# Optimization experiments

Hardware: AMD Instinct MI355X
Metric: run time of the kernel (lower is better)

Reference implementation:

```python
import jax, jax.numpy as jnp
import numpy as np
from jax import lax

A_NUM = 3
STRIDES = (4, 8, 16, 32, 64)
LEVEL_HW = ((128, 208), (64, 104), (32, 52), (16, 26), (8, 13))
IMG_H, IMG_W = 512.0, 832.0
PRE_NMS, POST_NMS, NMS_TH = 6000, 1000, 0.7


def _base_anchors(base_size, ratios=(0.5, 1.0, 2.0), scales=(8.0,)):
    ratios = np.asarray(ratios, np.float64)
    scales = np.asarray(scales, np.float64)
    cx = cy = (base_size - 1) / 2.0
    size = float(base_size) * float(base_size)
    ws = np.round(np.sqrt(size / ratios))
    hs = np.round(ws * ratios)
    ws = (ws[:, None] * scales[None, :]).reshape(-1)
    hs = (hs[:, None] * scales[None, :]).reshape(-1)
    return np.stack([cx - 0.5 * (ws - 1), cy - 0.5 * (hs - 1),
                     cx + 0.5 * (ws - 1), cy + 0.5 * (hs - 1)], axis=1)


def _all_anchors():
    # generate_anchors_global: per-level shifted grids, concatenated, order (h, w, a)
    out = []
    for stride, (h, w) in zip(STRIDES, LEVEL_HW):
        base = _base_anchors(stride)  # [A,4]
        sx = np.arange(w) * stride
        sy = np.arange(h) * stride
        sx, sy = np.meshgrid(sx, sy)
        shifts = np.stack([sx.ravel(), sy.ravel(), sx.ravel(), sy.ravel()], axis=1)
        anc = (shifts[:, None, :] + base[None, :, :]).reshape(-1, 4)  # [H*W*A,4]
        out.append(anc)
    return np.concatenate(out, axis=0).astype(np.float32)

_ANCHORS = _all_anchors()


def _conv(x, w, b, pad):
    y = lax.conv_general_dilated(x, w, (1, 1), [(pad, pad), (pad, pad)],
                                 dimension_numbers=('NCHW', 'OIHW', 'NCHW'))
    return y + b[None, :, None, None]


def _bbox_transform_inv(anchors, deltas):
    w = anchors[:, 2] - anchors[:, 0] + 1.0
    h = anchors[:, 3] - anchors[:, 1] + 1.0
    cx = anchors[:, 0] + 0.5 * w
    cy = anchors[:, 1] + 0.5 * h
    dx, dy, dw, dh = deltas[:, 0], deltas[:, 1], deltas[:, 2], deltas[:, 3]
    pcx = dx * w + cx
    pcy = dy * h + cy
    pw = jnp.exp(dw) * w
    ph = jnp.exp(dh) * h
    return jnp.stack([pcx - 0.5 * pw, pcy - 0.5 * ph,
                      pcx + 0.5 * pw, pcy + 0.5 * ph], axis=1)


def _iou_one_to_many(box, boxes):
    area = (boxes[:, 2] - boxes[:, 0] + 1.0) * (boxes[:, 3] - boxes[:, 1] + 1.0)
    area_b = (box[2] - box[0] + 1.0) * (box[3] - box[1] + 1.0)
    xx1 = jnp.maximum(box[0], boxes[:, 0])
    yy1 = jnp.maximum(box[1], boxes[:, 1])
    xx2 = jnp.minimum(box[2], boxes[:, 2])
    yy2 = jnp.minimum(box[3], boxes[:, 3])
    iw = jnp.maximum(0.0, xx2 - xx1 + 1.0)
    ih = jnp.maximum(0.0, yy2 - yy1 + 1.0)
    inter = iw * ih
    return inter / (area + area_b - inter)


def _nms_fixed(boxes, scores, thresh, max_out):
    # greedy NMS with a fixed number of iterations (jit-friendly)
    def body(s, _):
        i = jnp.argmax(s)
        valid = s[i] > -jnp.inf
        ious = _iou_one_to_many(boxes[i], boxes)
        s2 = jnp.where(ious > thresh, -jnp.inf, s)
        s2 = s2.at[i].set(-jnp.inf)
        return s2, (i, valid)
    _, (idx, valid) = lax.scan(body, scores, None, length=max_out)
    return idx, valid


def _rpn_forward(feats, im_info, rpn_conv_w, rpn_conv_b, rpn_score_w,
                 rpn_score_b, rpn_bbox_w, rpn_bbox_b):
    fg_scores, bbox_deltas = [], []
    for p in feats:
        H, W = p.shape[-2], p.shape[-1]
        f = _conv(p, rpn_conv_w, rpn_conv_b, 1)              # [1,512,H,W]
        cls = _conv(f, rpn_score_w, rpn_score_b, 0)          # [1,2A,H,W]
        # _reshape_layer(.,2) + softmax(dim=1) + _reshape_layer back + permute
        prob = jax.nn.softmax(cls.reshape(1, 2, A_NUM, H, W), axis=1)
        prob = prob.reshape(1, 2 * A_NUM, H, W).transpose(0, 2, 3, 1)  # [1,H,W,2A]
        fg = prob[..., A_NUM:].reshape(-1)                    # fg prob, order (h,w,a)
        bb = _conv(f, rpn_bbox_w, rpn_bbox_b, 0).transpose(0, 2, 3, 1).reshape(-1, 4)
        fg_scores.append(fg)
        bbox_deltas.append(bb)
    scores = jnp.concatenate(fg_scores, axis=0)              # [Ntot]
    deltas = jnp.concatenate(bbox_deltas, axis=0)            # [Ntot,4]
    anchors = jnp.asarray(_ANCHORS)

    proposals = _bbox_transform_inv(anchors, deltas)
    # clip to image
    proposals = jnp.stack([
        jnp.clip(proposals[:, 0], 0.0, im_info[1] - 1.0),
        jnp.clip(proposals[:, 1], 0.0, im_info[0] - 1.0),
        jnp.clip(proposals[:, 2], 0.0, im_info[1] - 1.0),
        jnp.clip(proposals[:, 3], 0.0, im_info[0] - 1.0)], axis=1)

    # pre-NMS top-k by score
    top_scores, order = lax.top_k(scores, PRE_NMS)
    top_boxes = proposals[order]
    keep, valid = _nms_fixed(top_boxes, top_scores, NMS_TH, POST_NMS)
    vmask = valid.astype(top_boxes.dtype)[:, None]
    sel_boxes = top_boxes[keep] * vmask
    sel_scores = top_scores[keep][:, None] * vmask
    rois = jnp.concatenate([jnp.zeros((POST_NMS, 1), sel_boxes.dtype), sel_boxes], axis=1)
    return jnp.concatenate([rois, sel_scores], axis=1)        # [POST_NMS, 6]


def setup_inputs() -> dict:
    key = jax.random.key(0)
    ks = jax.random.split(key, 12)
    chans = 256
    feats = {}
    for i, (name, (h, w)) in enumerate(zip(['p2', 'p3', 'p4', 'p5', 'p6'], LEVEL_HW)):
        feats[name] = jax.random.normal(ks[i], (1, chans, h, w), jnp.float32)
    inp = dict(feats)
    inp['im_info'] = jnp.array([IMG_H, IMG_W, 1.0], jnp.float32)
    inp['rpn_conv_w'] = jax.random.normal(ks[5], (512, chans, 3, 3), jnp.float32) * 0.03
    inp['rpn_conv_b'] = jnp.zeros((512,), jnp.float32)
    inp['rpn_score_w'] = jax.random.normal(ks[6], (2 * A_NUM, 512, 1, 1), jnp.float32) * 0.03
    inp['rpn_score_b'] = jnp.zeros((2 * A_NUM,), jnp.float32)
    inp['rpn_bbox_w'] = jax.random.normal(ks[7], (4 * A_NUM, 512, 1, 1), jnp.float32) * 0.01
    inp['rpn_bbox_b'] = jnp.zeros((4 * A_NUM,), jnp.float32)
    return inp


def reference(p2, p3, p4, p5, p6, im_info, rpn_conv_w, rpn_conv_b,
              rpn_score_w, rpn_score_b, rpn_bbox_w, rpn_bbox_b):
    return _rpn_forward([p2, p3, p4, p5, p6], im_info, rpn_conv_w, rpn_conv_b,
                        rpn_score_w, rpn_score_b, rpn_bbox_w, rpn_bbox_b)
```

## Files before the change

kernel.cpp:

```cpp
#include <hip/hip_runtime.h>
#include <stdint.h>

#define N_ANCH   106392
#define PRE_NMS  6000
#define POST_NMS 1000
#define POOL_CAP 8192
#define NMS_BLKS 94
#define SUP_W    96

static __device__ const int    LV_H[5]      = {128, 64, 32, 16, 8};
static __device__ const int    LV_W[5]      = {208, 104, 52, 26, 13};
static __device__ const int    LV_STRIDE[5] = {4, 8, 16, 32, 64};
static __device__ const int    LV_PIX[5]    = {26624, 6656, 1664, 416, 104};
static __device__ const int    LV_TILE0[6]  = {0, 416, 520, 546, 553, 555};
static __device__ const int    LV_AOFF[6]   = {0, 79872, 99840, 104832, 106080, 106392};
static __device__ const int    GPOFF[6]     = {0, 26624, 33280, 34944, 35360, 35464};
static __device__ const double BASE_ANCH[5][3][4] = {
  {{-22.,-10.,25.,13.},   {-14.,-14.,17.,17.},    {-10.,-22.,13.,25.}},
  {{-40.,-20.,47.,27.},   {-28.,-28.,35.,35.},    {-20.,-44.,27.,51.}},
  {{-84.,-40.,99.,55.},   {-56.,-56.,71.,71.},    {-36.,-80.,51.,95.}},
  {{-164.,-72.,195.,103.},{-112.,-112.,143.,143.},{-76.,-168.,107.,199.}},
  {{-332.,-152.,395.,215.},{-224.,-224.,287.,287.},{-148.,-328.,211.,391.}}
};

__device__ __forceinline__ uint32_t sort32f(float f) {
  uint32_t u = __float_as_uint(f);
  return ((int)u < 0) ? ~u : (u | 0x80000000u);
}
__device__ __forceinline__ uint64_t sort64(double d) {
  uint64_t u = (uint64_t)__double_as_longlong(d);
  return ((long long)u < 0) ? ~u : (u | 0x8000000000000000ull);
}

__device__ __forceinline__ double combf(const float* sw, const float* bw, int c, int j) {
  if (j < 3) return (double)sw[(3 + j) * 512 + c] - (double)sw[j * 512 + c];
  return (double)bw[(j - 3) * 512 + c];
}

__global__ __launch_bounds__(256) void k_weff_part(const float* __restrict__ cw,
                                                   const float* __restrict__ sw,
                                                   const float* __restrict__ bw,
                                                   double* __restrict__ Wpart) {
  int chunk = blockIdx.x / 9;
  int tb = blockIdx.x % 9;
  int t = tb * 256 + threadIdx.x;
  int c0 = chunk * 32;
  double acc[15];
#pragma unroll
  for (int j = 0; j < 15; ++j) acc[j] = 0.0;
#pragma unroll 1
  for (int c = c0; c < c0 + 32; ++c) {
    double v = (double)cw[c * 2304 + t];
#pragma unroll
    for (int j = 0; j < 15; ++j) acc[j] += v * combf(sw, bw, c, j);
  }
  double* o = Wpart + (((size_t)chunk * 2304 + t) << 4);
#pragma unroll
  for (int j = 0; j < 15; ++j) o[j] = acc[j];
  o[15] = 0.0;
}

__global__ __launch_bounds__(256) void k_weff_fin(const double* __restrict__ Wpart,
                                                  const float* __restrict__ cb,
                                                  const float* __restrict__ sb,
                                                  const float* __restrict__ bb,
                                                  const float* __restrict__ sw,
                                                  const float* __restrict__ bw,
                                                  double* __restrict__ Weff,
                                                  double* __restrict__ fb,
                                                  float4* __restrict__ w3,
                                                  float* __restrict__ fb32) {
  if (blockIdx.x == 9) {
    __shared__ double ps[15][16];
    int tid = threadIdx.x;
    if (tid < 240) {
      int j = tid >> 4, part = tid & 15;
      double s = 0.0;
      for (int c = part * 32; c < part * 32 + 32; ++c)
        s += (double)cb[c] * combf(sw, bw, c, j);
      ps[j][part] = s;
    }
    __syncthreads();
    if (tid < 15) {
      double s = 0.0;
#pragma unroll
      for (int part = 0; part < 16; ++part) s += ps[tid][part];
      s += (tid < 3) ? ((double)sb[3 + tid] - (double)sb[tid]) : (double)bb[tid - 3];
      fb[tid] = s;
      if (tid < 3) fb32[tid] = (float)s;
    }
    if (tid == 15) fb32[3] = 0.f;
    return;
  }
  int t = blockIdx.x * 256 + threadIdx.x;
  double acc[15];
#pragma unroll
  for (int j = 0; j < 15; ++j) acc[j] = 0.0;
#pragma unroll 1
  for (int chunk = 0; chunk < 16; ++chunk) {
    const double* p = Wpart + (((size_t)chunk * 2304 + t) << 4);
#pragma unroll
    for (int j = 0; j < 15; ++j) acc[j] += p[j];
  }
  double* o = Weff + ((size_t)t << 4);
#pragma unroll
  for (int j = 0; j < 15; ++j) o[j] = acc[j];
  o[15] = 0.0;
  float4 wf;
  wf.x = (float)acc[0]; wf.y = (float)acc[1]; wf.z = (float)acc[2]; wf.w = 0.f;
  w3[t] = wf;
}

__device__ __forceinline__ void load9(float v[9], const float* __restrict__ ib,
                                      const bool rok[3], const bool cok[3],
                                      const int roff[3]) {
#pragma unroll
  for (int ky = 0; ky < 3; ++ky)
#pragma unroll
    for (int kx = 0; kx < 3; ++kx)
      v[ky * 3 + kx] = (rok[ky] && cok[kx]) ? ib[roff[ky] + kx] : 0.0f;
}

__global__ __launch_bounds__(256) void k_fast(
    const float* __restrict__ p0, const float* __restrict__ p1,
    const float* __restrict__ p2, const float* __restrict__ p3,
    const float* __restrict__ p4,
    const float4* __restrict__ w3, const float* __restrict__ fb32,
    float* __restrict__ logits32, uint32_t* __restrict__ hist) {
  __shared__ float4 w3s[2304];
  __shared__ float red[4][64][3];
  int tid = threadIdx.x, wv = tid >> 6, ln = tid & 63;
  for (int i = tid; i < 2304; i += 256) w3s[i] = w3[i];
  int t = blockIdx.x;
  int L = 0;
  while (L < 4 && t >= LV_TILE0[L + 1]) ++L;
  const float* inL = (L == 0) ? p0 : (L == 1) ? p1 : (L == 2) ? p2 : (L == 3) ? p3 : p4;
  int H = LV_H[L], W = LV_W[L], HW = H * W, PIX = LV_PIX[L];
  int pix = (t - LV_TILE0[L]) * 64 + ln;
  bool valid = pix < PIX;
  if (!valid) pix = PIX - 1;
  int h = pix / W, w = pix % W;
  bool rok[3], cok[3];
  int roff[3];
#pragma unroll
  for (int ky = 0; ky < 3; ++ky) {
    int iy = h + ky - 1;
    rok[ky] = (iy >= 0 && iy < H);
    roff[ky] = iy * W + w - 1;
  }
#pragma unroll
  for (int kx = 0; kx < 3; ++kx) {
    int ix = w + kx - 1;
    cok[kx] = (ix >= 0 && ix < W);
  }
  __syncthreads();
  float a0 = 0.f, a1 = 0.f, a2 = 0.f;
  int ci0 = wv * 64;
  const float* ib = inL + ci0 * HW;
#pragma unroll 1
  for (int ci = ci0; ci < ci0 + 64; ++ci, ib += HW) {
    float v[9];
    load9(v, ib, rok, cok, roff);
    const float4* wr = w3s + ci * 9;
#pragma unroll
    for (int t9 = 0; t9 < 9; ++t9) {
      float4 wt = wr[t9];
      float vv = v[t9];
      a0 += vv * wt.x; a1 += vv * wt.y; a2 += vv * wt.z;
    }
  }
  red[wv][ln][0] = a0; red[wv][ln][1] = a1; red[wv][ln][2] = a2;
  __syncthreads();
  if (wv == 0 && valid) {
    int gbase = LV_AOFF[L] + pix * 3;
#pragma unroll
    for (int a = 0; a < 3; ++a) {
      float f = (red[0][ln][a] + red[1][ln][a]) + (red[2][ln][a] + red[3][ln][a]);
      f += fb32[a];
      logits32[gbase + a] = f;
      atomicAdd(&hist[sort32f(f) >> 16], 1u);
    }
  }
}

__global__ __launch_bounds__(1024) void k_edge(const uint32_t* __restrict__ hist,
                                               uint32_t* __restrict__ cnts) {
  __shared__ uint32_t cs[1024];
  __shared__ uint32_t g_grp, g_suf;
  int t = threadIdx.x, wv = t >> 6, ln = t & 63;
#pragma unroll 4
  for (int r = 0; r < 64; ++r) {
    int g = r * 16 + wv;
    uint32_t x = hist[g * 64 + ln];
#pragma unroll
    for (int off = 32; off > 0; off >>= 1) x += __shfl_down(x, off);
    if (ln == 0) cs[g] = x;
  }
  __syncthreads();
  for (int off = 1; off < 1024; off <<= 1) {
    uint32_t v = cs[t] + ((t + off < 1024) ? cs[t + off] : 0u);
    __syncthreads();
    cs[t] = v;
    __syncthreads();
  }
  uint32_t sufnext = (t < 1023) ? cs[t + 1] : 0u;
  if (cs[t] >= PRE_NMS && sufnext < PRE_NMS) {
    g_grp = (uint32_t)t;
    g_suf = sufnext;
  }
  __syncthreads();
  if (t < 64) {
    uint32_t grp = g_grp, suf = g_suf;
    uint32_t x = hist[grp * 64 + t];
    uint32_t S = x;
#pragma unroll
    for (int off = 1; off < 64; off <<= 1) {
      uint32_t y = __shfl_down(S, off);
      if (t + off < 64) S += y;
    }
    unsigned long long mask = __ballot(suf + S >= PRE_NMS);
    int hi = 63 - (int)__clzll(mask);
    if (t == hi) {
      uint32_t e = grp * 64 + (uint32_t)hi;
      cnts[1] = (e > 2) ? e - 2 : 0;
    }
  }
}

__global__ __launch_bounds__(256) void k_compact(const float* __restrict__ logits32,
                                                 uint32_t* __restrict__ cnts,
                                                 uint32_t* __restrict__ alist) {
  int i = blockIdx.x * 256 + threadIdx.x;
  if (i >= N_ANCH) return;
  if ((sort32f(logits32[i]) >> 16) >= cnts[1]) {
    uint32_t pos = atomicAdd(&cnts[0], 1u);
    if (pos < POOL_CAP) alist[pos] = (uint32_t)i;
  }
}

__global__ __launch_bounds__(256) void k_refine(
    const float* __restrict__ p0, const float* __restrict__ p1,
    const float* __restrict__ p2, const float* __restrict__ p3,
    const float* __restrict__ p4,
    const double* __restrict__ Weff, const double* __restrict__ fb,
    const uint32_t* __restrict__ alist, const uint32_t* __restrict__ cnts,
    double* __restrict__ logits, double* __restrict__ deltas,
    uint64_t* __restrict__ pkey) {
  __shared__ double red[4][64][5];
  int tid = threadIdx.x, wv = tid >> 6, ln = tid & 63;
  int cnt = (int)cnts[0];
  if (cnt > POOL_CAP) cnt = POOL_CAP;
  int base = blockIdx.x * 64;
  if (base >= cnt) return;
  int slot = base + ln;
  if (slot >= cnt) slot = cnt - 1;
  int gi = (int)alist[slot];
  int gpix = gi / 3, a = gi - gpix * 3;
  int L = 0;
  while (L < 4 && gpix >= GPOFF[L + 1]) ++L;
  int pix = gpix - GPOFF[L];
  const float* inL = (L == 0) ? p0 : (L == 1) ? p1 : (L == 2) ? p2 : (L == 3) ? p3 : p4;
  int H = LV_H[L], W = LV_W[L], HW = H * W;
  int h = pix / W, w = pix % W;
  bool rok[3], cok[3];
  int roff[3];
#pragma unroll
  for (int ky = 0; ky < 3; ++ky) {
    int iy = h + ky - 1;
    rok[ky] = (iy >= 0 && iy < H);
    roff[ky] = iy * W + w - 1;
  }
#pragma unroll
  for (int kx = 0; kx < 3; ++kx) {
    int ix = w + kx - 1;
    cok[kx] = (ix >= 0 && ix < W);
  }
  double sc = 0.0, d0 = 0.0, d1 = 0.0, d2 = 0.0, d3 = 0.0;
  int js = a, jd = 3 + 4 * a;
  int ci0 = wv * 64;
  const float* ib = inL + ci0 * HW;
#pragma unroll 1
  for (int ci = ci0; ci < ci0 + 64; ++ci, ib += HW) {
    float v[9];
    load9(v, ib, rok, cok, roff);
    const double* wr = Weff + ((size_t)ci * 144);
#pragma unroll
    for (int t9 = 0; t9 < 9; ++t9) {
      double vd = (double)v[t9];
      const double* wt = wr + t9 * 16;
      sc += vd * wt[js];
      d0 += vd * wt[jd + 0];
      d1 += vd * wt[jd + 1];
      d2 += vd * wt[jd + 2];
      d3 += vd * wt[jd + 3];
    }
  }
  red[wv][ln][0] = sc;
  red[wv][ln][1] = d0; red[wv][ln][2] = d1;
  red[wv][ln][3] = d2; red[wv][ln][4] = d3;
  __syncthreads();
  if (wv == 0) {
    double f[5];
#pragma unroll
    for (int j = 0; j < 5; ++j)
      f[j] = red[0][ln][j] + red[1][ln][j] + red[2][ln][j] + red[3][ln][j];
    double lg = f[0] + fb[js];
    logits[gi] = lg;
    deltas[gi * 4 + 0] = f[1] + fb[jd + 0];
    deltas[gi * 4 + 1] = f[2] + fb[jd + 1];
    deltas[gi * 4 + 2] = f[3] + fb[jd + 2];
    deltas[gi * 4 + 3] = f[4] + fb[jd + 3];
    pkey[slot] = (sort64(lg) & ~0x1FFFFull) | (uint64_t)(0x1FFFFu - (uint32_t)gi);
  }
}

__global__ __launch_bounds__(256) void k_rank_cnt(const uint32_t* __restrict__ cnts,
                                                  const uint64_t* __restrict__ pkey,
                                                  uint32_t* __restrict__ rank32) {
  __shared__ uint64_t lk[512];
  int t = threadIdx.x;
  int cnt = (int)cnts[0];
  if (cnt > POOL_CAP) cnt = POOL_CAP;
  int it = blockIdx.x >> 4, jc = blockIdx.x & 15;
  int e = it * 256 + t;
  int c0 = jc * 512;
  if (it * 256 >= cnt || c0 >= cnt) return;
  int lim = cnt - c0; if (lim > 512) lim = 512;
  for (int i = t; i < 512; i += 256) lk[i] = (i < lim) ? pkey[c0 + i] : 0ull;
  __syncthreads();
  bool active = e < cnt;
  uint64_t mykey = active ? pkey[e] : ~0ull;
  int r = 0;
#pragma unroll 8
  for (int j = 0; j < 512; ++j) r += (lk[j] > mykey) ? 1 : 0;
  if (active && r) atomicAdd(&rank32[e], (uint32_t)r);
}

__global__ __launch_bounds__(256) void k_scatter(const uint32_t* __restrict__ cnts,
                                                 const uint64_t* __restrict__ pkey,
                                                 const uint32_t* __restrict__ rank32,
                                                 const double* __restrict__ logits,
                                                 const double* __restrict__ deltas,
                                                 const float* __restrict__ im_info,
                                                 double* __restrict__ ss,
                                                 double* __restrict__ sbx,
                                                 float4* __restrict__ bxf,
                                                 float* __restrict__ areaf) {
  int t = threadIdx.x;
  int cnt = (int)cnts[0];
  if (cnt > POOL_CAP) cnt = POOL_CAP;
  int e = blockIdx.x * 256 + t;
  if (blockIdx.x * 256 >= cnt) return;
  if (e >= cnt) return;
  int rank = (int)rank32[e];
  if (rank >= PRE_NMS) return;
  uint64_t mykey = pkey[e];
  int gi = 0x1FFFF - (int)(mykey & 0x1FFFFull);
  int L = 0;
  while (L < 4 && gi >= LV_AOFF[L + 1]) ++L;
  int rel = gi - LV_AOFF[L];
  int pix = rel / 3, a = rel % 3;
  int W = LV_W[L];
  int h = pix / W, w = pix % W;
  double imW1 = (double)im_info[1] - 1.0;
  double imH1 = (double)im_info[0] - 1.0;
  double shx = (double)(w * LV_STRIDE[L]), shy = (double)(h * LV_STRIDE[L]);
  double ax1 = BASE_ANCH[L][a][0] + shx, ay1 = BASE_ANCH[L][a][1] + shy;
  double ax2 = BASE_ANCH[L][a][2] + shx, ay2 = BASE_ANCH[L][a][3] + shy;
  double dx = deltas[gi * 4 + 0], dy = deltas[gi * 4 + 1];
  double dw = deltas[gi * 4 + 2], dh = deltas[gi * 4 + 3];
  double wa = ax2 - ax1 + 1.0, ha = ay2 - ay1 + 1.0;
  double cx = ax1 + 0.5 * wa, cy = ay1 + 0.5 * ha;
  double pcx = dx * wa + cx, pcy = dy * ha + cy;
  double pw = exp(dw) * wa, ph = exp(dh) * ha;
  double x1 = fmin(fmax(pcx - 0.5 * pw, 0.0), imW1);
  double y1 = fmin(fmax(pcy - 0.5 * ph, 0.0), imH1);
  double x2 = fmin(fmax(pcx + 0.5 * pw, 0.0), imW1);
  double y2 = fmin(fmax(pcy + 0.5 * ph, 0.0), imH1);
  ss[rank] = 1.0 / (1.0 + exp(-logits[gi]));
  sbx[rank * 4 + 0] = x1; sbx[rank * 4 + 1] = y1;
  sbx[rank * 4 + 2] = x2; sbx[rank * 4 + 3] = y2;
  float4 bf;
  bf.x = (float)x1; bf.y = (float)y1; bf.z = (float)x2; bf.w = (float)y2;
  bxf[rank] = bf;
  areaf[rank] = (float)((x2 - x1 + 1.0) * (y2 - y1 + 1.0));
}

__device__ __forceinline__ bool iou_gt(const double* A, const double* B) {
  double areaA = (A[2] - A[0] + 1.0) * (A[3] - A[1] + 1.0);
  double areaB = (B[2] - B[0] + 1.0) * (B[3] - B[1] + 1.0);
  double xx1 = fmax(A[0], B[0]), yy1 = fmax(A[1], B[1]);
  double xx2 = fmin(A[2], B[2]), yy2 = fmin(A[3], B[3]);
  double iw = fmax(0.0, xx2 - xx1 + 1.0), ih = fmax(0.0, yy2 - yy1 + 1.0);
  double inter = iw * ih;
  return inter > 0.7 * (areaA + areaB - inter);
}

__global__ __launch_bounds__(256) void k_build(const double* __restrict__ sbx,
                                               const float4* __restrict__ bxf,
                                               const float* __restrict__ areaf,
                                               uint64_t* __restrict__ Sup) {
  __shared__ float cbx[256][5];
  __shared__ float rbx[64][5];
  int blk = blockIdx.x;
  int rtile = blk / 24, ctile = blk % 24;
  int t = threadIdx.x, q = t >> 6, ln = t & 63;
  int r = rtile * 64 + ln;
  int w = ctile * 4 + q;
  {
    int c = ctile * 256 + t;
    float4 b;
    float ar;
    if (c < NMS_BLKS * 64) { b = bxf[c]; ar = areaf[c]; }
    else { b.x = b.y = b.z = b.w = 0.f; ar = 0.f; }
    cbx[t][0] = b.x; cbx[t][1] = b.y; cbx[t][2] = b.z; cbx[t][3] = b.w; cbx[t][4] = ar;
    if (t < 64) {
      int rr = rtile * 64 + t;
      float4 rb = bxf[rr];
      rbx[t][0] = rb.x; rbx[t][1] = rb.y; rbx[t][2] = rb.z; rbx[t][3] = rb.w;
      rbx[t][4] = areaf[rr];
    }
  }
  __syncthreads();
  uint64_t bits = 0ull;
  int j0 = w * 64;
  if (w < NMS_BLKS && j0 + 63 > r) {
    float ax1 = rbx[ln][0], ay1 = rbx[ln][1], ax2 = rbx[ln][2], ay2 = rbx[ln][3];
    float aar = rbx[ln][4];
#pragma unroll 4
    for (int jj = 0; jj < 64; ++jj) {
      int j = j0 + jj;
      if (j <= r) continue;
      int cl = q * 64 + jj;
      float iw = fminf(ax2, cbx[cl][2]) - fmaxf(ax1, cbx[cl][0]) + 1.f;
      float ih = fminf(ay2, cbx[cl][3]) - fmaxf(ay1, cbx[cl][1]) + 1.f;
      float inter = fmaxf(iw, 0.f) * fmaxf(ih, 0.f);
      float d = inter - 0.7f * (aar + cbx[cl][4] - inter);
      bool sup;
      if (d > 4.0f) sup = true;
      else if (d < -4.0f) sup = false;
      else sup = iou_gt(sbx + (size_t)r * 4, sbx + (size_t)j * 4);
      if (sup) bits |= 1ull << jj;
    }
  }
  Sup[(size_t)r * SUP_W + w] = bits;
}

__global__ __launch_bounds__(256) void k_scan(const uint64_t* __restrict__ Sup,
                                              const double* __restrict__ ss,
                                              const double* __restrict__ sbx,
                                              float* __restrict__ out) {
  __shared__ uint16_t keep[POST_NMS];
  __shared__ uint64_t wpart[4];
  __shared__ uint64_t s_ext;
  __shared__ int kcnt;
  int t = threadIdx.x, wv = t >> 6, ln = t & 63;
  if (t == 0) kcnt = 0;
  __syncthreads();
  for (int b = 0; b < NMS_BLKS; ++b) {
    int base = b * 64;
    int K = kcnt;
    uint64_t m = 0ull;
    for (int p = t; p < K; p += 256) m |= Sup[(size_t)keep[p] * SUP_W + b];
#pragma unroll
    for (int off = 32; off > 0; off >>= 1) m |= __shfl_down(m, off);
    if (ln == 0) wpart[wv] = m;
    __syncthreads();
    if (t == 0) s_ext = wpart[0] | wpart[1] | wpart[2] | wpart[3];
    __syncthreads();
    if (wv == 0) {
      uint64_t myrow = Sup[(size_t)(base + ln) * SUP_W + b] & ~((2ull << ln) - 1ull);
      uint64_t ext = s_ext;
      if (base + 63 >= PRE_NMS) {
        int v = PRE_NMS - base;
        ext |= ~((1ull << v) - 1ull);
      }
      uint64_t avail = ~ext;
      uint64_t kp = 0ull;
      int K0 = kcnt, lim = POST_NMS - K0, nk = 0;
      while (avail && nk < lim) {
        int i2 = __ffsll((unsigned long long)avail) - 1;
        kp |= 1ull << i2;
        ++nk;
        uint64_t row = __shfl(myrow, i2);
        avail &= ~row;
        avail &= ~(1ull << i2);
      }
      if ((kp >> ln) & 1ull) {
        int pos = K0 + __popcll(kp & ((1ull << ln) - 1ull));
        keep[pos] = (uint16_t)(base + ln);
      }
      if (ln == 0) kcnt = K0 + nk;
    }
    __syncthreads();
    if (kcnt >= POST_NMS) break;
  }
  __syncthreads();
  int KF = kcnt;
  for (int r = t; r < POST_NMS; r += 256) {
    float* o = out + r * 6;
    if (r < KF) {
      int p = keep[r];
      o[0] = 0.f;
      o[1] = (float)sbx[p * 4 + 0];
      o[2] = (float)sbx[p * 4 + 1];
      o[3] = (float)sbx[p * 4 + 2];
      o[4] = (float)sbx[p * 4 + 3];
      o[5] = (float)ss[p];
    } else {
#pragma unroll
      for (int c = 0; c < 6; ++c) o[c] = 0.f;
    }
  }
}

extern "C" void kernel_launch(void* const* d_in, const int* in_sizes, int n_in,
                              void* d_out, int out_size, void* d_ws, size_t ws_size,
                              hipStream_t stream) {
  const float* p0 = (const float*)d_in[0];
  const float* p1 = (const float*)d_in[1];
  const float* p2 = (const float*)d_in[2];
  const float* p3 = (const float*)d_in[3];
  const float* p4 = (const float*)d_in[4];
  const float* im_info = (const float*)d_in[5];
  const float* cw = (const float*)d_in[6];
  const float* cb = (const float*)d_in[7];
  const float* sw = (const float*)d_in[8];
  const float* sb = (const float*)d_in[9];
  const float* bw = (const float*)d_in[10];
  const float* bb = (const float*)d_in[11];
  char* ws = (char*)d_ws;
  uint32_t* hist    = (uint32_t*)(ws + 0);
  uint32_t* cnts    = (uint32_t*)(ws + 262144);
  double*   fb      = (double*)  (ws + 262208);
  float*    fb32    = (float*)   (ws + 262336);
  double*   logits  = (double*)  (ws + 262352);
  double*   deltas  = (double*)  (ws + 1113488);
  float*    logits32= (float*)   (ws + 4518032);
  float4*   w3      = (float4*)  (ws + 4943600);
  double*   Weff    = (double*)  (ws + 4980464);
  double*   Wpart   = (double*)  (ws + 5275376);
  uint32_t* alist   = (uint32_t*)(ws + 9993968);
  double*   ssort   = (double*)  (ws + 10026736);
  double*   sbx     = (double*)  (ws + 10074864);
  float4*   bxf     = (float4*)  (ws + 10267376);
  float*    areaf   = (float*)   (ws + 10363632);
  uint64_t* Sup     = (uint64_t*)(ws + 10387696);
  uint64_t* pkey    = (uint64_t*)(ws + 15007984);
  uint32_t* rank32  = (uint32_t*)(ws + 15073520);
  float* out = (float*)d_out;

  hipMemsetAsync(ws, 0, 262208, stream);
  hipMemsetAsync(rank32, 0, 32768, stream);
  k_weff_part<<<144, 256, 0, stream>>>(cw, sw, bw, Wpart);
  k_weff_fin<<<10, 256, 0, stream>>>(Wpart, cb, sb, bb, sw, bw, Weff, fb, w3, fb32);
  k_fast<<<555, 256, 0, stream>>>(p0, p1, p2, p3, p4, w3, fb32, logits32, hist);
  k_edge<<<1, 1024, 0, stream>>>(hist, cnts);
  k_compact<<<416, 256, 0, stream>>>(logits32, cnts, alist);
  k_refine<<<128, 256, 0, stream>>>(p0, p1, p2, p3, p4, Weff, fb, alist, cnts,
                                    logits, deltas, pkey);
  k_rank_cnt<<<512, 256, 0, stream>>>(cnts, pkey, rank32);
  k_scatter<<<32, 256, 0, stream>>>(cnts, pkey, rank32, logits, deltas, im_info,
                                    ssort, sbx, bxf, areaf);
  k_build<<<94 * 24, 256, 0, stream>>>(sbx, bxf, areaf, Sup);
  k_scan<<<1, 256, 0, stream>>>(Sup, ssort, sbx, out);
}
```

Before: 500.7 us.

## Accumulate NMS suppression masks incrementally in shared memory during scan

The serial NMS scan kernel used to OR suppression rows from every kept box for each 64-box block, re-reading rows once per block. It now ORs only the rows of newly kept boxes into a shared-memory mask covering all later blocks, using shared atomics, and prefetches the next diagonal row block. This cuts the global reads from roughly quadratic to linear in kept boxes, at the cost of shared atomics and integer divisions in the loop.

```diff
diff --git a/kernel.cpp b/kernel.cpp
--- a/kernel.cpp
+++ b/kernel.cpp
@@ -451,33 +451,29 @@
                                               const double* __restrict__ sbx,
                                               float* __restrict__ out) {
   __shared__ uint16_t keep[POST_NMS];
-  __shared__ uint64_t wpart[4];
-  __shared__ uint64_t s_ext;
-  __shared__ int kcnt;
+  __shared__ uint32_t sup32[NMS_BLKS * 2];
+  __shared__ int s_kcnt, s_K0, s_nk;
   int t = threadIdx.x, wv = t >> 6, ln = t & 63;
-  if (t == 0) kcnt = 0;
+  for (int i = t; i < NMS_BLKS * 2; i += 256) sup32[i] = 0u;
+  if (t == 0) { s_kcnt = 0; s_K0 = 0; s_nk = 0; }
+  uint64_t nrow = 0ull;
+  if (wv == 0) nrow = Sup[(size_t)ln * SUP_W];
   __syncthreads();
   for (int b = 0; b < NMS_BLKS; ++b) {
-    int base = b * 64;
-    int K = kcnt;
-    uint64_t m = 0ull;
-    for (int p = t; p < K; p += 256) m |= Sup[(size_t)keep[p] * SUP_W + b];
-#pragma unroll
-    for (int off = 32; off > 0; off >>= 1) m |= __shfl_down(m, off);
-    if (ln == 0) wpart[wv] = m;
-    __syncthreads();
-    if (t == 0) s_ext = wpart[0] | wpart[1] | wpart[2] | wpart[3];
-    __syncthreads();
     if (wv == 0) {
-      uint64_t myrow = Sup[(size_t)(base + ln) * SUP_W + b] & ~((2ull << ln) - 1ull);
-      uint64_t ext = s_ext;
+      uint64_t myrow = nrow & ~((2ull << ln) - 1ull);
+      if (b + 1 < NMS_BLKS)
+        nrow = Sup[(size_t)((b + 1) * 64 + ln) * SUP_W + (b + 1)];
+      uint64_t ext = ((uint64_t)sup32[2 * b + 1] << 32) | sup32[2 * b];
+      int base = b * 64;
       if (base + 63 >= PRE_NMS) {
         int v = PRE_NMS - base;
         ext |= ~((1ull << v) - 1ull);
       }
+      int K0 = s_kcnt;
       uint64_t avail = ~ext;
       uint64_t kp = 0ull;
-      int K0 = kcnt, lim = POST_NMS - K0, nk = 0;
+      int lim = POST_NMS - K0, nk = 0;
       while (avail && nk < lim) {
         int i2 = __ffsll((unsigned long long)avail) - 1;
         kp |= 1ull << i2;
@@ -490,13 +486,40 @@
         int pos = K0 + __popcll(kp & ((1ull << ln) - 1ull));
         keep[pos] = (uint16_t)(base + ln);
       }
-      if (ln == 0) kcnt = K0 + nk;
+      if (ln == 0) { s_K0 = K0; s_nk = nk; s_kcnt = K0 + nk; }
     }
     __syncthreads();
-    if (kcnt >= POST_NMS) break;
-  }
-  __syncthreads();
-  int KF = kcnt;
+    int nk = s_nk, K0s = s_K0;
+    int rem = NMS_BLKS - 1 - b;
+    if (nk > 0 && rem > 0) {
+      int totalp = nk * rem;
+      for (int p0 = t; p0 < totalp; p0 += 1024) {
+        uint64_t v[4];
+        int wq[4];
+#pragma unroll
+        for (int u = 0; u < 4; ++u) {
+          int p = p0 + u * 256;
+          if (p < totalp) {
+            int ki = p / rem;
+            int w = b + 1 + (p - ki * rem);
+            wq[u] = w;
+            v[u] = Sup[(size_t)keep[K0s + ki] * SUP_W + w];
+          } else { wq[u] = -1; v[u] = 0ull; }
+        }
+#pragma unroll
+        for (int u = 0; u < 4; ++u) {
+          if (wq[u] >= 0 && v[u]) {
+            uint32_t lo = (uint32_t)v[u], hi = (uint32_t)(v[u] >> 32);
+            if (lo) atomicOr(&sup32[2 * wq[u]], lo);
+            if (hi) atomicOr(&sup32[2 * wq[u] + 1], hi);
+          }
+        }
+      }
+    }
+    __syncthreads();
+    if (s_kcnt >= POST_NMS) break;
+  }
+  int KF = s_kcnt;
   for (int r = t; r < POST_NMS; r += 256) {
     float* o = out + r * 6;
     if (r < KF) {
```

Result: slower. 550.1 us (+9.9%).

## Run NMS scan in a single wavefront with register-held suppression mask

Applied to the files above, without the earlier changes.

The greedy NMS scan now runs entirely in wave 0. Each lane keeps the OR of suppression words for the kept boxes in two 64-bit registers covering all column blocks. This replaces the per-block re-gather over all kept rows, the cross-wave shuffle reduction and two block barriers per iteration. The next diagonal row is prefetched, and after each block the newly kept rows are ORed into the running mask. The cost is a serial per-kept-box global load loop on one wave, with the other three waves idle.

```diff
diff --git a/kernel.cpp b/kernel.cpp
--- a/kernel.cpp
+++ b/kernel.cpp
@@ -451,33 +451,25 @@
                                               const double* __restrict__ sbx,
                                               float* __restrict__ out) {
   __shared__ uint16_t keep[POST_NMS];
-  __shared__ uint64_t wpart[4];
-  __shared__ uint64_t s_ext;
-  __shared__ int kcnt;
+  __shared__ int s_kcnt;
   int t = threadIdx.x, wv = t >> 6, ln = t & 63;
-  if (t == 0) kcnt = 0;
-  __syncthreads();
-  for (int b = 0; b < NMS_BLKS; ++b) {
-    int base = b * 64;
-    int K = kcnt;
-    uint64_t m = 0ull;
-    for (int p = t; p < K; p += 256) m |= Sup[(size_t)keep[p] * SUP_W + b];
-#pragma unroll
-    for (int off = 32; off > 0; off >>= 1) m |= __shfl_down(m, off);
-    if (ln == 0) wpart[wv] = m;
-    __syncthreads();
-    if (t == 0) s_ext = wpart[0] | wpart[1] | wpart[2] | wpart[3];
-    __syncthreads();
-    if (wv == 0) {
-      uint64_t myrow = Sup[(size_t)(base + ln) * SUP_W + b] & ~((2ull << ln) - 1ull);
-      uint64_t ext = s_ext;
+  if (wv == 0) {
+    uint64_t supw0 = 0ull, supw1 = 0ull;
+    uint64_t nrow = Sup[(size_t)ln * SUP_W];
+    int kcnt = 0;
+    for (int b = 0; b < NMS_BLKS && kcnt < POST_NMS; ++b) {
+      uint64_t myrow = nrow & ~((2ull << ln) - 1ull);
+      if (b + 1 < NMS_BLKS)
+        nrow = Sup[(size_t)((b + 1) * 64 + ln) * SUP_W + (b + 1)];
+      uint64_t ext = (b < 64) ? __shfl(supw0, b) : __shfl(supw1, b - 64);
+      int base = b * 64;
       if (base + 63 >= PRE_NMS) {
         int v = PRE_NMS - base;
         ext |= ~((1ull << v) - 1ull);
       }
       uint64_t avail = ~ext;
       uint64_t kp = 0ull;
-      int K0 = kcnt, lim = POST_NMS - K0, nk = 0;
+      int lim = POST_NMS - kcnt, nk = 0;
       while (avail && nk < lim) {
         int i2 = __ffsll((unsigned long long)avail) - 1;
         kp |= 1ull << i2;
@@ -487,16 +479,23 @@
         avail &= ~(1ull << i2);
       }
       if ((kp >> ln) & 1ull) {
-        int pos = K0 + __popcll(kp & ((1ull << ln) - 1ull));
+        int pos = kcnt + __popcll(kp & ((1ull << ln) - 1ull));
         keep[pos] = (uint16_t)(base + ln);
       }
-      if (ln == 0) kcnt = K0 + nk;
-    }
-    __syncthreads();
-    if (kcnt >= POST_NMS) break;
-  }
-  __syncthreads();
-  int KF = kcnt;
+      kcnt += nk;
+      uint64_t kpi = kp;
+      while (kpi) {
+        int j = __ffsll((unsigned long long)kpi) - 1;
+        kpi &= kpi - 1;
+        const uint64_t* rp = Sup + (size_t)(base + j) * SUP_W;
+        supw0 |= rp[ln];
+        if (ln < NMS_BLKS - 64) supw1 |= rp[64 + ln];
+      }
+    }
+    if (ln == 0) s_kcnt = kcnt;
+  }
+  __syncthreads();
+  int KF = s_kcnt;
   for (int r = t; r < POST_NMS; r += 256) {
     float* o = out + r * 6;
     if (r < KF) {
```

Measured after the change: 782.8 us. 1.56x slower.

## Widen NMS scan block and prefetch diagonal suppression rows

Applied to the files above, without the earlier changes.

The single-block NMS scan now runs with 1024 threads. Wave 0 prefetches the next block's diagonal Sup row while it resolves the current block. The OR of kept rows' masks for the next block is combined with shared-memory atomicOr into a per-block external mask, which removes one barrier and the serial wave-partial reduction per iteration. This targets the latency of the serial scan, at the cost of more threads contending on the barrier and shared atomics.

```diff
diff --git a/kernel.cpp b/kernel.cpp
--- a/kernel.cpp
+++ b/kernel.cpp
@@ -446,38 +446,34 @@
   Sup[(size_t)r * SUP_W + w] = bits;
 }
 
-__global__ __launch_bounds__(256) void k_scan(const uint64_t* __restrict__ Sup,
-                                              const double* __restrict__ ss,
-                                              const double* __restrict__ sbx,
-                                              float* __restrict__ out) {
+__global__ __launch_bounds__(1024) void k_scan(const uint64_t* __restrict__ Sup,
+                                               const double* __restrict__ ss,
+                                               const double* __restrict__ sbx,
+                                               float* __restrict__ out) {
   __shared__ uint16_t keep[POST_NMS];
-  __shared__ uint64_t wpart[4];
-  __shared__ uint64_t s_ext;
-  __shared__ int kcnt;
+  __shared__ uint32_t ext_arr[NMS_BLKS][2];
+  __shared__ int s_kcnt;
   int t = threadIdx.x, wv = t >> 6, ln = t & 63;
-  if (t == 0) kcnt = 0;
+  for (int i = t; i < NMS_BLKS * 2; i += 1024) ext_arr[i >> 1][i & 1] = 0u;
+  if (t == 0) s_kcnt = 0;
+  uint64_t nrow = 0ull;
+  if (wv == 0) nrow = Sup[(size_t)ln * SUP_W];
   __syncthreads();
   for (int b = 0; b < NMS_BLKS; ++b) {
-    int base = b * 64;
-    int K = kcnt;
-    uint64_t m = 0ull;
-    for (int p = t; p < K; p += 256) m |= Sup[(size_t)keep[p] * SUP_W + b];
-#pragma unroll
-    for (int off = 32; off > 0; off >>= 1) m |= __shfl_down(m, off);
-    if (ln == 0) wpart[wv] = m;
-    __syncthreads();
-    if (t == 0) s_ext = wpart[0] | wpart[1] | wpart[2] | wpart[3];
-    __syncthreads();
     if (wv == 0) {
-      uint64_t myrow = Sup[(size_t)(base + ln) * SUP_W + b] & ~((2ull << ln) - 1ull);
-      uint64_t ext = s_ext;
+      uint64_t myrow = nrow & ~((2ull << ln) - 1ull);
+      if (b + 1 < NMS_BLKS)
+        nrow = Sup[(size_t)((b + 1) * 64 + ln) * SUP_W + (b + 1)];
+      uint64_t ext = ((uint64_t)ext_arr[b][1] << 32) | ext_arr[b][0];
+      int base = b * 64;
       if (base + 63 >= PRE_NMS) {
         int v = PRE_NMS - base;
         ext |= ~((1ull << v) - 1ull);
       }
+      int K0 = s_kcnt;
       uint64_t avail = ~ext;
       uint64_t kp = 0ull;
-      int K0 = kcnt, lim = POST_NMS - K0, nk = 0;
+      int lim = POST_NMS - K0, nk = 0;
       while (avail && nk < lim) {
         int i2 = __ffsll((unsigned long long)avail) - 1;
         kp |= 1ull << i2;
@@ -490,14 +486,25 @@
         int pos = K0 + __popcll(kp & ((1ull << ln) - 1ull));
         keep[pos] = (uint16_t)(base + ln);
       }
-      if (ln == 0) kcnt = K0 + nk;
+      if (ln == 0) s_kcnt = K0 + nk;
     }
     __syncthreads();
-    if (kcnt >= POST_NMS) break;
-  }
-  __syncthreads();
-  int KF = kcnt;
-  for (int r = t; r < POST_NMS; r += 256) {
+    int K = s_kcnt;
+    if (K >= POST_NMS || b + 1 >= NMS_BLKS) break;
+    uint64_t m = 0ull;
+    for (int p = t; p < K; p += 1024) m |= Sup[(size_t)keep[p] * SUP_W + (b + 1)];
+#pragma unroll
+    for (int off = 32; off > 0; off >>= 1) m |= __shfl_down(m, off);
+    if (ln == 0 && m) {
+      uint32_t lo = (uint32_t)m, hi = (uint32_t)(m >> 32);
+      if (lo) atomicOr(&ext_arr[b + 1][0], lo);
+      if (hi) atomicOr(&ext_arr[b + 1][1], hi);
+    }
+    __syncthreads();
+  }
+  __syncthreads();
+  int KF = s_kcnt;
+  for (int r = t; r < POST_NMS; r += 1024) {
     float* o = out + r * 6;
     if (r < KF) {
       int p = keep[r];
@@ -563,5 +570,5 @@
   k_scatter<<<32, 256, 0, stream>>>(cnts, pkey, rank32, logits, deltas, im_info,
                                     ssort, sbx, bxf, areaf);
   k_build<<<94 * 24, 256, 0, stream>>>(sbx, bxf, areaf, Sup);
-  k_scan<<<1, 256, 0, stream>>>(Sup, ssort, sbx, out);
-}
+  k_scan<<<1, 1024, 0, stream>>>(Sup, ssort, sbx, out);
+}
```

Measured after the change: 492.5 us. Within noise of the previous version (-1.6%).
